# Performance work log

Measured on AMD Instinct MI355X. Metric: run time of the kernel, lower is better.

Reference implementation:

```python
import jax, jax.numpy as jnp
import numpy as np
import math

B, S, D, H = 4, 1024, 1024, 16
DK = D // H


def setup_inputs() -> dict:
    key = jax.random.key(0)
    ks = jax.random.split(key, 12)
    inp = {
        "q": jax.random.normal(ks[0], (B, S, D), jnp.float32),
        "k": jax.random.normal(ks[1], (B, S, D), jnp.float32),
        "v": jax.random.normal(ks[2], (B, S, D), jnp.float32),
        # causal mask, broadcast over batch (0 = masked)
        "mask": jnp.broadcast_to(jnp.tril(jnp.ones((S, S), jnp.int32)), (B, S, S)),
    }
    sc = 1.0 / math.sqrt(D)
    # torch nn.Linear convention: y = x @ W.T + b, W:[out,in]
    inp["Wq"] = jax.random.normal(ks[3], (D, D), jnp.float32) * sc
    inp["bq"] = jnp.zeros((D,), jnp.float32)
    inp["Wk"] = jax.random.normal(ks[4], (D, D), jnp.float32) * sc
    inp["bk"] = jnp.zeros((D,), jnp.float32)
    inp["Wv"] = jax.random.normal(ks[5], (D, D), jnp.float32) * sc
    inp["bv"] = jnp.zeros((D,), jnp.float32)
    inp["Wo"] = jax.random.normal(ks[6], (D, D), jnp.float32) * sc
    inp["bo"] = jnp.zeros((D,), jnp.float32)
    return inp


def _mha(q, k, v, mask, Wq, bq, Wk, bk, Wv, bv, Wo, bo):
    def split_heads(x):  # [B,S,D] -> [B,H,S,DK]
        return x.reshape(B, S, H, DK).transpose(0, 2, 1, 3)

    qh = split_heads(q @ Wq.T + bq)
    kh = split_heads(k @ Wk.T + bk)
    vh = split_heads(v @ Wv.T + bv)

    scores = jnp.einsum("bhqd,bhkd->bhqk", qh, kh) / math.sqrt(DK)
    scores = jnp.where(mask[:, None, :, :] == 0, jnp.float32(-1e9), scores)
    weights = jax.nn.softmax(scores, axis=-1)  # dropout in eval mode -> identity
    out = jnp.einsum("bhqk,bhkd->bhqd", weights, vh)
    out = out.transpose(0, 2, 1, 3).reshape(B, S, D)
    return out @ Wo.T + bo


def reference(q, k, v, mask, Wq, bq, Wk, bk, Wv, bv, Wo, bo):
    return _mha(q, k, v, mask, Wq, bq, Wk, bk, Wv, bv, Wo, bo)
```

## Files before the change

### kernel.cpp

```cpp
#include <hip/hip_runtime.h>

typedef unsigned short u16;
typedef __bf16 bf16x8 __attribute__((ext_vector_type(8)));
typedef float floatx4 __attribute__((ext_vector_type(4)));
typedef unsigned short ush8 __attribute__((ext_vector_type(8)));

#define BB 4
#define SS 1024
#define DD 1024
#define HH 16
#define DKK 64
#define MM (BB*SS)

__device__ __forceinline__ u16 f2bf(float f) {
    union { float f; unsigned int u; } v; v.f = f;
    unsigned int r = v.u + 0x7fffu + ((v.u >> 16) & 1u);
    return (u16)(r >> 16);
}

__device__ __forceinline__ void async16(const u16* g, u16* l) {
    __builtin_amdgcn_global_load_lds(
        (const __attribute__((address_space(1))) void*)g,
        (__attribute__((address_space(3))) void*)l,
        16, 0, 0);
}

__global__ __launch_bounds__(256) void convert_kernel(
    const float* __restrict__ q, const float* __restrict__ k, const float* __restrict__ v,
    const float* __restrict__ Wq, const float* __restrict__ Wk, const float* __restrict__ Wv,
    const float* __restrict__ Wo,
    u16* qb, u16* kb, u16* vb, u16* Wqb, u16* Wkb, u16* Wvb, u16* Wob) {
    const int Q4 = (BB*SS*DD) / 4;
    const int W4 = (DD*DD) / 4;
    int idx = blockIdx.x * 256 + threadIdx.x;
    const float* src; u16* dst; int off;
    if (idx < Q4)            { src = q; dst = qb; off = idx; }
    else if (idx < 2*Q4)     { src = k; dst = kb; off = idx - Q4; }
    else if (idx < 3*Q4)     { src = v; dst = vb; off = idx - 2*Q4; }
    else {
        int r = idx - 3*Q4;
        int wsel = r / W4; off = r - wsel*W4;
        src = wsel==0 ? Wq : wsel==1 ? Wk : wsel==2 ? Wv : Wo;
        dst = wsel==0 ? Wqb : wsel==1 ? Wkb : wsel==2 ? Wvb : Wob;
    }
    float4 x = ((const float4*)src)[off];
    ushort4 y;
    y.x = f2bf(x.x); y.y = f2bf(x.y); y.z = f2bf(x.z); y.w = f2bf(x.w);
    ((ushort4*)dst)[off] = y;
}

__global__ __launch_bounds__(256) void qkv_gemm(
    const u16* __restrict__ qb, const u16* __restrict__ kb, const u16* __restrict__ vb,
    const u16* __restrict__ Wqb, const u16* __restrict__ Wkb, const u16* __restrict__ Wvb,
    const float* __restrict__ bq, const float* __restrict__ bk, const float* __restrict__ bv,
    u16* Qh, u16* Kh, u16* Vh) {
    const int K = DD;
    __shared__ u16 sA[128*32];
    __shared__ u16 sW[128*32];
    int nb = blockIdx.x;
    int m0 = blockIdx.y * 128;
    int which = nb >> 3;
    int n0 = (nb & 7) * 128;
    const u16* A   = which==0 ? qb  : which==1 ? kb  : vb;
    const u16* W   = which==0 ? Wqb : which==1 ? Wkb : Wvb;
    const float* bias = which==0 ? bq : which==1 ? bk : bv;
    u16* Out = which==0 ? Qh : which==1 ? Kh : Vh;
    float scale = which==0 ? 0.125f : 1.0f;

    int t = threadIdx.x;
    int w = t >> 6, l = t & 63, g = l >> 4, c = l & 15;
    int wm = w & 1, wn = w >> 1;

    floatx4 acc[4][4] = {};

    int srow = t >> 2, sseg = t & 3;
    const u16* gA0 = A + (m0 + srow) * K + sseg*8;
    const u16* gW0 = W + (n0 + srow) * K + sseg*8;
    u16* lA = &sA[t*8];
    u16* lW = &sW[t*8];

    for (int kk = 0; kk < K; kk += 32) {
        __syncthreads();
        async16(gA0 + kk,          lA);
        async16(gA0 + 64*K + kk,   lA + 64*32);
        async16(gW0 + kk,          lW);
        async16(gW0 + 64*K + kk,   lW + 64*32);
        __syncthreads();
        bf16x8 af[4], bf_[4];
        #pragma unroll
        for (int i = 0; i < 4; i++) af[i]  = *(const bf16x8*)&sA[(wm*64 + i*16 + c)*32 + g*8];
        #pragma unroll
        for (int j = 0; j < 4; j++) bf_[j] = *(const bf16x8*)&sW[(wn*64 + j*16 + c)*32 + g*8];
        #pragma unroll
        for (int i = 0; i < 4; i++)
            #pragma unroll
            for (int j = 0; j < 4; j++)
                acc[i][j] = __builtin_amdgcn_mfma_f32_16x16x32_bf16(af[i], bf_[j], acc[i][j], 0, 0, 0);
    }

    #pragma unroll
    for (int j = 0; j < 4; j++) {
        int col = n0 + wn*64 + j*16 + c;
        float bb = bias[col];
        int h = col >> 6, dk = col & 63;
        #pragma unroll
        for (int i = 0; i < 4; i++) {
            #pragma unroll
            for (int r = 0; r < 4; r++) {
                int row = m0 + wm*64 + i*16 + g*4 + r;
                int b = row >> 10, s = row & 1023;
                float vv = (acc[i][j][r] + bb) * scale;
                Out[((size_t)(b*HH + h)*SS + s)*DKK + dk] = f2bf(vv);
            }
        }
    }
}

__global__ __launch_bounds__(256) void attn_kernel(
    const u16* __restrict__ Qh, const u16* __restrict__ Kh, const u16* __restrict__ Vh,
    u16* __restrict__ attnO) {
    __shared__ u16 sQ[128*72];
    __shared__ u16 sK[64*72];
    __shared__ u16 sVt[64*72];
    __shared__ u16 sP[128*72];

    int q0 = blockIdx.x * 128;
    int bh = blockIdx.y;
    const u16* Qp = Qh + (size_t)bh * SS * DKK;
    const u16* Kp = Kh + (size_t)bh * SS * DKK;
    const u16* Vp = Vh + (size_t)bh * SS * DKK;

    int t = threadIdx.x, w = t >> 6, l = t & 63, g = l >> 4, c = l & 15;
    int wq = w * 32;

    #pragma unroll
    for (int i = 0; i < 4; i++) {
        int seg = t + i*256;
        int row = seg >> 3, sc = seg & 7;
        *(uint4*)&sQ[row*72 + sc*8] = *(const uint4*)&Qp[(q0 + row)*DKK + sc*8];
    }

    float m_[2][4], l_[2][4];
    floatx4 o[2][4] = {};
    #pragma unroll
    for (int mt = 0; mt < 2; mt++)
        #pragma unroll
        for (int r = 0; r < 4; r++) { m_[mt][r] = -3e38f; l_[mt][r] = 0.f; }

    int kend = q0 + 128;
    for (int k0 = 0; k0 < kend; k0 += 64) {
        __syncthreads();
        {
            int seg = t, row = seg >> 3, sc = seg & 7;
            *(uint4*)&sK[row*72 + sc*8] = *(const uint4*)&Kp[(k0 + row)*DKK + sc*8];
            seg = t + 256; row = seg >> 3; sc = seg & 7;
            *(uint4*)&sK[row*72 + sc*8] = *(const uint4*)&Kp[(k0 + row)*DKK + sc*8];
        }
        #pragma unroll
        for (int p = 0; p < 2; p++) {
            int dkb = w*8 + p*32;
            ush8 vv = *(const ush8*)&Vp[(k0 + l)*DKK + dkb];
            #pragma unroll
            for (int j = 0; j < 8; j++) sVt[(dkb + j)*72 + l] = vv[j];
        }
        __syncthreads();

        floatx4 sc_[2][4] = {};
        #pragma unroll
        for (int ks = 0; ks < 2; ks++) {
            bf16x8 aq[2], bk_[4];
            aq[0] = *(const bf16x8*)&sQ[(wq + c)*72 + ks*32 + g*8];
            aq[1] = *(const bf16x8*)&sQ[(wq + 16 + c)*72 + ks*32 + g*8];
            #pragma unroll
            for (int nt = 0; nt < 4; nt++)
                bk_[nt] = *(const bf16x8*)&sK[(nt*16 + c)*72 + ks*32 + g*8];
            #pragma unroll
            for (int mt = 0; mt < 2; mt++)
                #pragma unroll
                for (int nt = 0; nt < 4; nt++)
                    sc_[mt][nt] = __builtin_amdgcn_mfma_f32_16x16x32_bf16(aq[mt], bk_[nt], sc_[mt][nt], 0, 0, 0);
        }

        bool need_mask = (k0 >= q0);
        #pragma unroll
        for (int mt = 0; mt < 2; mt++) {
            if (need_mask) {
                #pragma unroll
                for (int nt = 0; nt < 4; nt++)
                    #pragma unroll
                    for (int r = 0; r < 4; r++) {
                        int qg = q0 + wq + mt*16 + g*4 + r;
                        int kg = k0 + nt*16 + c;
                        if (kg > qg) sc_[mt][nt][r] = -3e38f;
                    }
            }
            float rm[4];
            #pragma unroll
            for (int r = 0; r < 4; r++) {
                float vv = fmaxf(fmaxf(sc_[mt][0][r], sc_[mt][1][r]),
                                 fmaxf(sc_[mt][2][r], sc_[mt][3][r]));
                vv = fmaxf(vv, __shfl_xor(vv, 1));
                vv = fmaxf(vv, __shfl_xor(vv, 2));
                vv = fmaxf(vv, __shfl_xor(vv, 4));
                vv = fmaxf(vv, __shfl_xor(vv, 8));
                rm[r] = vv;
            }
            #pragma unroll
            for (int r = 0; r < 4; r++) {
                float mnew = fmaxf(m_[mt][r], rm[r]);
                float alpha = __expf(m_[mt][r] - mnew);
                m_[mt][r] = mnew;
                float rs = 0.f;
                #pragma unroll
                for (int nt = 0; nt < 4; nt++) {
                    float p = __expf(sc_[mt][nt][r] - mnew);
                    sc_[mt][nt][r] = p;
                    rs += p;
                }
                rs += __shfl_xor(rs, 1);
                rs += __shfl_xor(rs, 2);
                rs += __shfl_xor(rs, 4);
                rs += __shfl_xor(rs, 8);
                l_[mt][r] = l_[mt][r] * alpha + rs;
                #pragma unroll
                for (int nt = 0; nt < 4; nt++) o[mt][nt][r] *= alpha;
                #pragma unroll
                for (int nt = 0; nt < 4; nt++)
                    sP[(wq + mt*16 + g*4 + r)*72 + nt*16 + c] = f2bf(sc_[mt][nt][r]);
            }
        }

        #pragma unroll
        for (int ks = 0; ks < 2; ks++) {
            bf16x8 ap[2], bv_[4];
            ap[0] = *(const bf16x8*)&sP[(wq + c)*72 + ks*32 + g*8];
            ap[1] = *(const bf16x8*)&sP[(wq + 16 + c)*72 + ks*32 + g*8];
            #pragma unroll
            for (int nt = 0; nt < 4; nt++)
                bv_[nt] = *(const bf16x8*)&sVt[(nt*16 + c)*72 + ks*32 + g*8];
            #pragma unroll
            for (int mt = 0; mt < 2; mt++)
                #pragma unroll
                for (int nt = 0; nt < 4; nt++)
                    o[mt][nt] = __builtin_amdgcn_mfma_f32_16x16x32_bf16(ap[mt], bv_[nt], o[mt][nt], 0, 0, 0);
        }
    }

    int b = bh >> 4, h = bh & 15;
    #pragma unroll
    for (int mt = 0; mt < 2; mt++)
        #pragma unroll
        for (int r = 0; r < 4; r++) {
            float inv = 1.0f / l_[mt][r];
            int row = q0 + wq + mt*16 + g*4 + r;
            #pragma unroll
            for (int nt = 0; nt < 4; nt++) {
                int dcol = h*64 + nt*16 + c;
                attnO[((size_t)b*SS + row)*DD + dcol] = f2bf(o[mt][nt][r] * inv);
            }
        }
}

__global__ __launch_bounds__(256) void out_gemm(
    const u16* __restrict__ A, const u16* __restrict__ W,
    const float* __restrict__ bo, float* __restrict__ out) {
    const int K = DD;
    __shared__ u16 sA[128*32];
    __shared__ u16 sW[128*32];
    int n0 = blockIdx.x * 128;
    int m0 = blockIdx.y * 128;

    int t = threadIdx.x;
    int w = t >> 6, l = t & 63, g = l >> 4, c = l & 15;
    int wm = w & 1, wn = w >> 1;

    floatx4 acc[4][4] = {};

    int srow = t >> 2, sseg = t & 3;
    const u16* gA0 = A + (m0 + srow) * K + sseg*8;
    const u16* gW0 = W + (n0 + srow) * K + sseg*8;
    u16* lA = &sA[t*8];
    u16* lW = &sW[t*8];

    for (int kk = 0; kk < K; kk += 32) {
        __syncthreads();
        async16(gA0 + kk,        lA);
        async16(gA0 + 64*K + kk, lA + 64*32);
        async16(gW0 + kk,        lW);
        async16(gW0 + 64*K + kk, lW + 64*32);
        __syncthreads();
        bf16x8 af[4], bf_[4];
        #pragma unroll
        for (int i = 0; i < 4; i++) af[i]  = *(const bf16x8*)&sA[(wm*64 + i*16 + c)*32 + g*8];
        #pragma unroll
        for (int j = 0; j < 4; j++) bf_[j] = *(const bf16x8*)&sW[(wn*64 + j*16 + c)*32 + g*8];
        #pragma unroll
        for (int i = 0; i < 4; i++)
            #pragma unroll
            for (int j = 0; j < 4; j++)
                acc[i][j] = __builtin_amdgcn_mfma_f32_16x16x32_bf16(af[i], bf_[j], acc[i][j], 0, 0, 0);
    }

    #pragma unroll
    for (int j = 0; j < 4; j++) {
        int col = n0 + wn*64 + j*16 + c;
        float bb = bo[col];
        #pragma unroll
        for (int i = 0; i < 4; i++) {
            #pragma unroll
            for (int r = 0; r < 4; r++) {
                int row = m0 + wm*64 + i*16 + g*4 + r;
                out[(size_t)row*DD + col] = acc[i][j][r] + bb;
            }
        }
    }
}

extern "C" void kernel_launch(void* const* d_in, const int* in_sizes, int n_in,
                              void* d_out, int out_size, void* d_ws, size_t ws_size,
                              hipStream_t stream) {
    const float* q    = (const float*)d_in[0];
    const float* k    = (const float*)d_in[1];
    const float* v    = (const float*)d_in[2];
    const float* Wq   = (const float*)d_in[4];
    const float* bq   = (const float*)d_in[5];
    const float* Wk   = (const float*)d_in[6];
    const float* bk   = (const float*)d_in[7];
    const float* Wv   = (const float*)d_in[8];
    const float* bv   = (const float*)d_in[9];
    const float* Wo   = (const float*)d_in[10];
    const float* bo   = (const float*)d_in[11];
    float* out = (float*)d_out;

    char* ws = (char*)d_ws;
    const size_t MB = 1024*1024;
    u16* qb   = (u16*)(ws + 0*MB);
    u16* kb   = (u16*)(ws + 8*MB);
    u16* vb   = (u16*)(ws + 16*MB);
    u16* Wqb  = (u16*)(ws + 24*MB);
    u16* Wkb  = (u16*)(ws + 26*MB);
    u16* Wvb  = (u16*)(ws + 28*MB);
    u16* Wob  = (u16*)(ws + 30*MB);
    u16* Qh   = (u16*)(ws + 32*MB);
    u16* Kh   = (u16*)(ws + 40*MB);
    u16* Vh   = (u16*)(ws + 48*MB);
    u16* attn = (u16*)(ws + 56*MB);

    convert_kernel<<<16384, 256, 0, stream>>>(q, k, v, Wq, Wk, Wv, Wo,
                                              qb, kb, vb, Wqb, Wkb, Wvb, Wob);
    qkv_gemm<<<dim3(24, 32), 256, 0, stream>>>(qb, kb, vb, Wqb, Wkb, Wvb,
                                               bq, bk, bv, Qh, Kh, Vh);
    attn_kernel<<<dim3(8, 64), 256, 0, stream>>>(Qh, Kh, Vh, attn);
    out_gemm<<<dim3(8, 32), 256, 0, stream>>>(attn, Wob, bo, out);
}
```

Measured before the change: 256.1 us.

## Write V pre-transposed from QKV GEMM and shrink attention query tiles to 64

The QKV projection now stores V in a [b,h,dk,s] transposed layout, so the attention kernel can load V tiles with vectorized 16-byte copies instead of scalar LDS transposes. The attention block handles 64 query rows (one 16-row tile per wave), which doubles the grid to 1024 blocks. Blocks are issued heaviest-first by reversing the query-tile index, to balance the causal workload. The transposed V store in the GEMM epilogue is strided and uncoalesced, and each wave does less MFMA work per K/V tile load.

```diff
diff --git a/kernel.cpp b/kernel.cpp
--- a/kernel.cpp
+++ b/kernel.cpp
@@ -3,7 +3,6 @@
 typedef unsigned short u16;
 typedef __bf16 bf16x8 __attribute__((ext_vector_type(8)));
 typedef float floatx4 __attribute__((ext_vector_type(4)));
-typedef unsigned short ush8 __attribute__((ext_vector_type(8)));
 
 #define BB 4
 #define SS 1024
@@ -53,7 +52,7 @@
     const u16* __restrict__ qb, const u16* __restrict__ kb, const u16* __restrict__ vb,
     const u16* __restrict__ Wqb, const u16* __restrict__ Wkb, const u16* __restrict__ Wvb,
     const float* __restrict__ bq, const float* __restrict__ bk, const float* __restrict__ bv,
-    u16* Qh, u16* Kh, u16* Vh) {
+    u16* Qh, u16* Kh, u16* Vt) {
     const int K = DD;
     __shared__ u16 sA[128*32];
     __shared__ u16 sW[128*32];
@@ -64,7 +63,7 @@
     const u16* A   = which==0 ? qb  : which==1 ? kb  : vb;
     const u16* W   = which==0 ? Wqb : which==1 ? Wkb : Wvb;
     const float* bias = which==0 ? bq : which==1 ? bk : bv;
-    u16* Out = which==0 ? Qh : which==1 ? Kh : Vh;
+    u16* Out = which==0 ? Qh : which==1 ? Kh : Vt;
     float scale = which==0 ? 0.125f : 1.0f;
 
     int t = threadIdx.x;
@@ -110,155 +109,132 @@
                 int row = m0 + wm*64 + i*16 + g*4 + r;
                 int b = row >> 10, s = row & 1023;
                 float vv = (acc[i][j][r] + bb) * scale;
-                Out[((size_t)(b*HH + h)*SS + s)*DKK + dk] = f2bf(vv);
+                u16 bits = f2bf(vv);
+                if (which == 2) {
+                    Out[((size_t)((b*HH + h)*DKK + dk))*SS + s] = bits;
+                } else {
+                    Out[((size_t)(b*HH + h)*SS + s)*DKK + dk] = bits;
+                }
             }
         }
     }
 }
 
 __global__ __launch_bounds__(256) void attn_kernel(
-    const u16* __restrict__ Qh, const u16* __restrict__ Kh, const u16* __restrict__ Vh,
+    const u16* __restrict__ Qh, const u16* __restrict__ Kh, const u16* __restrict__ Vt,
     u16* __restrict__ attnO) {
-    __shared__ u16 sQ[128*72];
+    __shared__ u16 sQ[64*72];
     __shared__ u16 sK[64*72];
     __shared__ u16 sVt[64*72];
-    __shared__ u16 sP[128*72];
-
-    int q0 = blockIdx.x * 128;
+    __shared__ u16 sP[64*72];
+
+    int qt = 15 - blockIdx.x;
+    int q0 = qt * 64;
     int bh = blockIdx.y;
-    const u16* Qp = Qh + (size_t)bh * SS * DKK;
-    const u16* Kp = Kh + (size_t)bh * SS * DKK;
-    const u16* Vp = Vh + (size_t)bh * SS * DKK;
+    const u16* Qp  = Qh + (size_t)bh * SS * DKK;
+    const u16* Kp  = Kh + (size_t)bh * SS * DKK;
+    const u16* Vtp = Vt + (size_t)bh * DKK * SS;
 
     int t = threadIdx.x, w = t >> 6, l = t & 63, g = l >> 4, c = l & 15;
-    int wq = w * 32;
-
-    #pragma unroll
-    for (int i = 0; i < 4; i++) {
-        int seg = t + i*256;
+    int wq = w * 16;
+
+    #pragma unroll
+    for (int p = 0; p < 2; p++) {
+        int seg = t + p*256;
         int row = seg >> 3, sc = seg & 7;
         *(uint4*)&sQ[row*72 + sc*8] = *(const uint4*)&Qp[(q0 + row)*DKK + sc*8];
     }
 
-    float m_[2][4], l_[2][4];
-    floatx4 o[2][4] = {};
-    #pragma unroll
-    for (int mt = 0; mt < 2; mt++)
-        #pragma unroll
-        for (int r = 0; r < 4; r++) { m_[mt][r] = -3e38f; l_[mt][r] = 0.f; }
-
-    int kend = q0 + 128;
-    for (int k0 = 0; k0 < kend; k0 += 64) {
-        __syncthreads();
-        {
-            int seg = t, row = seg >> 3, sc = seg & 7;
-            *(uint4*)&sK[row*72 + sc*8] = *(const uint4*)&Kp[(k0 + row)*DKK + sc*8];
-            seg = t + 256; row = seg >> 3; sc = seg & 7;
-            *(uint4*)&sK[row*72 + sc*8] = *(const uint4*)&Kp[(k0 + row)*DKK + sc*8];
-        }
+    float m_[4], l_[4];
+    floatx4 o[4] = {};
+    #pragma unroll
+    for (int r = 0; r < 4; r++) { m_[r] = -3e38f; l_[r] = 0.f; }
+
+    for (int k0 = 0; k0 <= q0; k0 += 64) {
+        __syncthreads();
         #pragma unroll
         for (int p = 0; p < 2; p++) {
-            int dkb = w*8 + p*32;
-            ush8 vv = *(const ush8*)&Vp[(k0 + l)*DKK + dkb];
-            #pragma unroll
-            for (int j = 0; j < 8; j++) sVt[(dkb + j)*72 + l] = vv[j];
-        }
-        __syncthreads();
-
-        floatx4 sc_[2][4] = {};
+            int seg = t + p*256;
+            int row = seg >> 3, sc = seg & 7;
+            *(uint4*)&sK[row*72 + sc*8]  = *(const uint4*)&Kp[(k0 + row)*DKK + sc*8];
+            *(uint4*)&sVt[row*72 + sc*8] = *(const uint4*)&Vtp[row*SS + k0 + sc*8];
+        }
+        __syncthreads();
+
+        floatx4 sc_[4] = {};
         #pragma unroll
         for (int ks = 0; ks < 2; ks++) {
-            bf16x8 aq[2], bk_[4];
-            aq[0] = *(const bf16x8*)&sQ[(wq + c)*72 + ks*32 + g*8];
-            aq[1] = *(const bf16x8*)&sQ[(wq + 16 + c)*72 + ks*32 + g*8];
+            bf16x8 aq = *(const bf16x8*)&sQ[(wq + c)*72 + ks*32 + g*8];
+            #pragma unroll
+            for (int nt = 0; nt < 4; nt++) {
+                bf16x8 bk_ = *(const bf16x8*)&sK[(nt*16 + c)*72 + ks*32 + g*8];
+                sc_[nt] = __builtin_amdgcn_mfma_f32_16x16x32_bf16(aq, bk_, sc_[nt], 0, 0, 0);
+            }
+        }
+
+        if (k0 == q0) {
             #pragma unroll
             for (int nt = 0; nt < 4; nt++)
-                bk_[nt] = *(const bf16x8*)&sK[(nt*16 + c)*72 + ks*32 + g*8];
-            #pragma unroll
-            for (int mt = 0; mt < 2; mt++)
                 #pragma unroll
-                for (int nt = 0; nt < 4; nt++)
-                    sc_[mt][nt] = __builtin_amdgcn_mfma_f32_16x16x32_bf16(aq[mt], bk_[nt], sc_[mt][nt], 0, 0, 0);
-        }
-
-        bool need_mask = (k0 >= q0);
-        #pragma unroll
-        for (int mt = 0; mt < 2; mt++) {
-            if (need_mask) {
-                #pragma unroll
-                for (int nt = 0; nt < 4; nt++)
-                    #pragma unroll
-                    for (int r = 0; r < 4; r++) {
-                        int qg = q0 + wq + mt*16 + g*4 + r;
-                        int kg = k0 + nt*16 + c;
-                        if (kg > qg) sc_[mt][nt][r] = -3e38f;
-                    }
-            }
-            float rm[4];
-            #pragma unroll
-            for (int r = 0; r < 4; r++) {
-                float vv = fmaxf(fmaxf(sc_[mt][0][r], sc_[mt][1][r]),
-                                 fmaxf(sc_[mt][2][r], sc_[mt][3][r]));
-                vv = fmaxf(vv, __shfl_xor(vv, 1));
-                vv = fmaxf(vv, __shfl_xor(vv, 2));
-                vv = fmaxf(vv, __shfl_xor(vv, 4));
-                vv = fmaxf(vv, __shfl_xor(vv, 8));
-                rm[r] = vv;
-            }
-            #pragma unroll
-            for (int r = 0; r < 4; r++) {
-                float mnew = fmaxf(m_[mt][r], rm[r]);
-                float alpha = __expf(m_[mt][r] - mnew);
-                m_[mt][r] = mnew;
-                float rs = 0.f;
-                #pragma unroll
-                for (int nt = 0; nt < 4; nt++) {
-                    float p = __expf(sc_[mt][nt][r] - mnew);
-                    sc_[mt][nt][r] = p;
-                    rs += p;
+                for (int r = 0; r < 4; r++) {
+                    int qg = wq + g*4 + r;
+                    int kg = nt*16 + c;
+                    if (kg > qg) sc_[nt][r] = -3e38f;
                 }
-                rs += __shfl_xor(rs, 1);
-                rs += __shfl_xor(rs, 2);
-                rs += __shfl_xor(rs, 4);
-                rs += __shfl_xor(rs, 8);
-                l_[mt][r] = l_[mt][r] * alpha + rs;
-                #pragma unroll
-                for (int nt = 0; nt < 4; nt++) o[mt][nt][r] *= alpha;
-                #pragma unroll
-                for (int nt = 0; nt < 4; nt++)
-                    sP[(wq + mt*16 + g*4 + r)*72 + nt*16 + c] = f2bf(sc_[mt][nt][r]);
-            }
+        }
+
+        #pragma unroll
+        for (int r = 0; r < 4; r++) {
+            float vv = fmaxf(fmaxf(sc_[0][r], sc_[1][r]), fmaxf(sc_[2][r], sc_[3][r]));
+            vv = fmaxf(vv, __shfl_xor(vv, 1));
+            vv = fmaxf(vv, __shfl_xor(vv, 2));
+            vv = fmaxf(vv, __shfl_xor(vv, 4));
+            vv = fmaxf(vv, __shfl_xor(vv, 8));
+            float mnew = fmaxf(m_[r], vv);
+            float alpha = __expf(m_[r] - mnew);
+            m_[r] = mnew;
+            float rs = 0.f;
+            #pragma unroll
+            for (int nt = 0; nt < 4; nt++) {
+                float p = __expf(sc_[nt][r] - mnew);
+                sc_[nt][r] = p;
+                rs += p;
+            }
+            rs += __shfl_xor(rs, 1);
+            rs += __shfl_xor(rs, 2);
+            rs += __shfl_xor(rs, 4);
+            rs += __shfl_xor(rs, 8);
+            l_[r] = l_[r] * alpha + rs;
+            #pragma unroll
+            for (int nt = 0; nt < 4; nt++) o[nt][r] *= alpha;
+            int prow = (wq + g*4 + r)*72;
+            #pragma unroll
+            for (int nt = 0; nt < 4; nt++)
+                sP[prow + nt*16 + c] = f2bf(sc_[nt][r]);
         }
 
         #pragma unroll
         for (int ks = 0; ks < 2; ks++) {
-            bf16x8 ap[2], bv_[4];
-            ap[0] = *(const bf16x8*)&sP[(wq + c)*72 + ks*32 + g*8];
-            ap[1] = *(const bf16x8*)&sP[(wq + 16 + c)*72 + ks*32 + g*8];
-            #pragma unroll
-            for (int nt = 0; nt < 4; nt++)
-                bv_[nt] = *(const bf16x8*)&sVt[(nt*16 + c)*72 + ks*32 + g*8];
-            #pragma unroll
-            for (int mt = 0; mt < 2; mt++)
-                #pragma unroll
-                for (int nt = 0; nt < 4; nt++)
-                    o[mt][nt] = __builtin_amdgcn_mfma_f32_16x16x32_bf16(ap[mt], bv_[nt], o[mt][nt], 0, 0, 0);
+            bf16x8 ap = *(const bf16x8*)&sP[(wq + c)*72 + ks*32 + g*8];
+            #pragma unroll
+            for (int nt = 0; nt < 4; nt++) {
+                bf16x8 bv_ = *(const bf16x8*)&sVt[(nt*16 + c)*72 + ks*32 + g*8];
+                o[nt] = __builtin_amdgcn_mfma_f32_16x16x32_bf16(ap, bv_, o[nt], 0, 0, 0);
+            }
         }
     }
 
     int b = bh >> 4, h = bh & 15;
     #pragma unroll
-    for (int mt = 0; mt < 2; mt++)
-        #pragma unroll
-        for (int r = 0; r < 4; r++) {
-            float inv = 1.0f / l_[mt][r];
-            int row = q0 + wq + mt*16 + g*4 + r;
-            #pragma unroll
-            for (int nt = 0; nt < 4; nt++) {
-                int dcol = h*64 + nt*16 + c;
-                attnO[((size_t)b*SS + row)*DD + dcol] = f2bf(o[mt][nt][r] * inv);
-            }
-        }
+    for (int r = 0; r < 4; r++) {
+        float inv = 1.0f / l_[r];
+        int row = q0 + wq + g*4 + r;
+        #pragma unroll
+        for (int nt = 0; nt < 4; nt++) {
+            int dcol = h*64 + nt*16 + c;
+            attnO[((size_t)b*SS + row)*DD + dcol] = f2bf(o[nt][r] * inv);
+        }
+    }
 }
 
 __global__ __launch_bounds__(256) void out_gemm(
@@ -343,13 +319,13 @@
     u16* Wob  = (u16*)(ws + 30*MB);
     u16* Qh   = (u16*)(ws + 32*MB);
     u16* Kh   = (u16*)(ws + 40*MB);
-    u16* Vh   = (u16*)(ws + 48*MB);
+    u16* Vt   = (u16*)(ws + 48*MB);
     u16* attn = (u16*)(ws + 56*MB);
 
     convert_kernel<<<16384, 256, 0, stream>>>(q, k, v, Wq, Wk, Wv, Wo,
                                               qb, kb, vb, Wqb, Wkb, Wvb, Wob);
     qkv_gemm<<<dim3(24, 32), 256, 0, stream>>>(qb, kb, vb, Wqb, Wkb, Wvb,
-                                               bq, bk, bv, Qh, Kh, Vh);
-    attn_kernel<<<dim3(8, 64), 256, 0, stream>>>(Qh, Kh, Vh, attn);
+                                               bq, bk, bv, Qh, Kh, Vt);
+    attn_kernel<<<dim3(16, 64), 256, 0, stream>>>(Qh, Kh, Vt, attn);
     out_gemm<<<dim3(8, 32), 256, 0, stream>>>(attn, Wob, bo, out);
 }
```

Result: slower. 261.5 us (+2.1%).
